# Performance work log

Hardware: AMD Instinct MI355X
Metric: run time of the kernel (lower is better)

Reference implementation:

```python
import jax, jax.numpy as jnp
import numpy as np

K = 16  # num_neighbors
L = 3   # stacked PointTransformer layers


def _mlp2(x, w1, b1, w2, b2):
    return jax.nn.relu(x @ w1 + b1) @ w2 + b2


def setup_inputs() -> dict:
    key = jax.random.key(0)
    ks = jax.random.split(key, 10)
    B, N, D = 2, 8192, 3
    HP, HA = 32, 12  # pos_mlp hidden, attn_mlp hidden (3*4)
    f = lambda k, shp, s: jax.random.normal(k, shp, dtype=jnp.float32) * s
    return {
        "feats": f(ks[0], (B, N, D), 1.0),
        "pos": f(ks[1], (B, N, 3), 1.0),
        "mask": jnp.ones((B, N), dtype=bool),  # unused by PT.forward
        "w_qkv": f(ks[2], (L, D, 3 * D), 1.0 / np.sqrt(D)),
        "pos_w1": f(ks[3], (L, 3, HP), 1.0 / np.sqrt(3.0)),
        "pos_b1": jnp.zeros((L, HP), jnp.float32),
        "pos_w2": f(ks[4], (L, HP, D), 1.0 / np.sqrt(HP)),
        "pos_b2": jnp.zeros((L, D), jnp.float32),
        "attn_w1": f(ks[5], (L, D, HA), 1.0 / np.sqrt(D)),
        "attn_b1": jnp.zeros((L, HA), jnp.float32),
        "attn_w2": f(ks[6], (L, HA, D), 1.0 / np.sqrt(HA)),
        "attn_b2": jnp.zeros((L, D), jnp.float32),
        "lin_w": f(ks[7], (D, 2), 1.0 / np.sqrt(D)),
        "lin_b": jnp.zeros((2,), jnp.float32),
    }


def reference(feats, pos, mask, w_qkv, pos_w1, pos_b1, pos_w2, pos_b2,
              attn_w1, attn_b1, attn_w2, attn_b2, lin_w, lin_b):
    # kNN indices from pairwise squared distances (monotonic in the norm the
    # original uses, so topk-smallest gives identical neighbor sets).
    sq = jnp.sum(pos * pos, axis=-1)                               # [B,N]
    d2 = sq[:, :, None] + sq[:, None, :] - 2.0 * jnp.einsum('bic,bjc->bij', pos, pos)
    _, idx = jax.lax.top_k(-d2, K)                                 # [B,N,K]

    gather = jax.vmap(lambda t, i: t[i])                           # [B,N,d],[B,N,K]->[B,N,K,d]
    pos_j = gather(pos, idx)                                       # [B,N,K,3]
    rel_pos = pos[:, :, None, :] - pos_j                           # [B,N,K,3]

    h = feats
    for l in range(L):
        qkv = h @ w_qkv[l]                                         # [B,N,9]
        q, k, v = jnp.split(qkv, 3, axis=-1)
        k_j = gather(k, idx)                                       # [B,N,K,3]
        v_j = gather(v, idx)
        rel_emb = _mlp2(rel_pos, pos_w1[l], pos_b1[l], pos_w2[l], pos_b2[l])
        qk_rel = q[:, :, None, :] - k_j
        sim = _mlp2(qk_rel + rel_emb, attn_w1[l], attn_b1[l], attn_w2[l], attn_b2[l])
        attn = jax.nn.softmax(sim, axis=-2)                        # softmax over neighbors
        agg = jnp.einsum('bijd,bijd->bid', attn, v_j + rel_emb)    # [B,N,3]
        h = jax.nn.sigmoid(agg)
    out = h @ lin_w + lin_b                                        # [B,N,2]
    return jax.nn.softmax(out, axis=2)
```

## Files before the change

kernel.cpp:

```cpp
#include <hip/hip_runtime.h>
#include <math.h>

#define N_PTS 8192
#define BATCH 2
#define KNB 16
#define NQ (BATCH * N_PTS)

#define H    0.35f
#define INVH (1.0f / 0.35f)
#define NC   30
#define LBOX (0.5f * H * NC)
#define NCELL (NC * NC * NC)
#define MCELL (2 * NCELL)
#define RMAXF 2
#define NCHK 8
#define CHKP (N_PTS / NCHK)
#define SCANG 8192
#define MERGG 1024
#define WCAP 8192

typedef unsigned long long u64;

__device__ __forceinline__ float med3f(float a, float b, float c) {
#if __has_builtin(__builtin_amdgcn_fmed3f)
    return __builtin_amdgcn_fmed3f(a, b, c);
#else
    return fmaxf(fminf(a, b), fminf(fmaxf(a, b), c));
#endif
}

__device__ __forceinline__ unsigned sortable(float x) {
    unsigned u = __float_as_uint(x);
    return u ^ ((unsigned)((int)u >> 31) | 0x80000000u);
}

__device__ __forceinline__ void ins_u64(u64 (&pk)[KNB], u64 key) {
    if (key < pk[0]) {
#pragma unroll
        for (int s = 0; s < KNB; ++s) {
            const u64 ds1 = (s < KNB - 1) ? pk[s + 1] : 0ull;
            const bool c0 = key < pk[s];
            const bool c1 = key < ds1;
            pk[s] = c1 ? ds1 : (c0 ? key : pk[s]);
        }
    }
}

__device__ __forceinline__ void sort16_desc_u64(u64 (&a)[KNB]) {
#pragma unroll
    for (int k = 2; k <= 16; k <<= 1) {
#pragma unroll
        for (int j = k >> 1; j > 0; j >>= 1) {
#pragma unroll
            for (int i = 0; i < 16; ++i) {
                const int l = i ^ j;
                if (l > i) {
                    const bool dirDesc = ((i & k) == 0);
                    const u64 mx = a[i] > a[l] ? a[i] : a[l];
                    const u64 mn = a[i] > a[l] ? a[l] : a[i];
                    a[i] = dirDesc ? mx : mn;
                    a[l] = dirDesc ? mn : mx;
                }
            }
        }
    }
}

__device__ __forceinline__ void merge64_u64(u64 (&pk)[KNB]) {
#pragma unroll
    for (int mm = 1; mm <= 32; mm <<= 1) {
        u64 L[KNB];
#pragma unroll
        for (int i = 0; i < KNB; ++i) {
            const u64 a = pk[i];
            const u64 c = __shfl_xor(pk[KNB - 1 - i], mm);
            L[i] = a < c ? a : c;
        }
#pragma unroll
        for (int dd = 8; dd >= 1; dd >>= 1) {
#pragma unroll
            for (int i = 0; i < KNB; ++i) {
                if ((i & dd) == 0) {
                    const u64 hi = L[i] > L[i | dd] ? L[i] : L[i | dd];
                    const u64 lo = L[i] > L[i | dd] ? L[i | dd] : L[i];
                    L[i] = hi; L[i | dd] = lo;
                }
            }
        }
#pragma unroll
        for (int i = 0; i < KNB; ++i) pk[i] = L[i];
    }
}

__global__ __launch_bounds__(256) void kzero(int* __restrict__ p, int n) {
    const int i = blockIdx.x * 256 + threadIdx.x;
    if (i < n) p[i] = 0;
}

__global__ __launch_bounds__(256) void kcount(const float* __restrict__ pos,
                                              int* __restrict__ cnt,
                                              int* __restrict__ cellid) {
    const int g = blockIdx.x * 256 + threadIdx.x;
    const int b = g >> 13;
    const float x = pos[g * 3 + 0], y = pos[g * 3 + 1], z = pos[g * 3 + 2];
    int cx = (int)floorf((x + LBOX) * INVH); cx = min(max(cx, 0), NC - 1);
    int cy = (int)floorf((y + LBOX) * INVH); cy = min(max(cy, 0), NC - 1);
    int cz = (int)floorf((z + LBOX) * INVH); cz = min(max(cz, 0), NC - 1);
    const int c = (((b * NC) + cz) * NC + cy) * NC + cx;
    cellid[g] = c;
    atomicAdd(&cnt[c], 1);
}

__global__ __launch_bounds__(1024) void kscan1(const int* __restrict__ cnt,
                                               int* __restrict__ scanned,
                                               int* __restrict__ bsum) {
    __shared__ int sh[1024];
    const int t = threadIdx.x;
    const int idx = blockIdx.x * 1024 + t;
    int v = (idx < MCELL) ? cnt[idx] : 0;
    sh[t] = v;
    __syncthreads();
    for (int off = 1; off < 1024; off <<= 1) {
        const int add = (t >= off) ? sh[t - off] : 0;
        __syncthreads();
        sh[t] += add;
        __syncthreads();
    }
    if (idx < MCELL) scanned[idx] = sh[t];
    if (t == 1023) bsum[blockIdx.x] = sh[1023];
}

__global__ __launch_bounds__(1024) void kscan2(const int* __restrict__ scanned,
                                               const int* __restrict__ bsum,
                                               int* __restrict__ cell_start) {
    __shared__ int soff;
    const int t = threadIdx.x;
    const int blk = blockIdx.x;
    const int idx = blk * 1024 + t;
    if (t == 0) {
        int s = 0;
        for (int k = 0; k < blk; ++k) s += bsum[k];
        soff = s;
    }
    __syncthreads();
    if (idx < MCELL) cell_start[idx + 1] = scanned[idx] + soff;
    if (idx == 0) cell_start[0] = 0;
}

__global__ __launch_bounds__(256) void kscatter(const float* __restrict__ pos,
                                                const int* __restrict__ cellid,
                                                const int* __restrict__ cell_start,
                                                int* __restrict__ cnt2,
                                                float4* __restrict__ spp,
                                                int* __restrict__ sidx) {
    const int g = blockIdx.x * 256 + threadIdx.x;
    const int c = cellid[g];
    const int off = atomicAdd(&cnt2[c], 1);
    const int p = cell_start[c] + off;
    const float x = pos[g * 3 + 0], y = pos[g * 3 + 1], z = pos[g * 3 + 2];
    spp[p] = make_float4(-2.f * x, -2.f * y, -2.f * z, fmaf(x, x, fmaf(y, y, z * z)));
    sidx[p] = g & (N_PTS - 1);
}

__global__ __launch_bounds__(64) void ksearch_fast(const float4* __restrict__ spp,
                                                   const int* __restrict__ sidx,
                                                   const int* __restrict__ cs,
                                                   int* __restrict__ knn,
                                                   int* __restrict__ ovf_list,
                                                   int* __restrict__ ovf_cnt) {
    const int tid = threadIdx.x;
    const int li  = tid & 15;
    const int sq  = blockIdx.x * 4 + (tid >> 4);
    const int b   = sq >> 13;

    const float4 me = spp[sq];
    const float qx = -0.5f * me.x, qy = -0.5f * me.y, qz = -0.5f * me.z;
    const float qsq = me.w;
    int cx = (int)floorf((qx + LBOX) * INVH); cx = min(max(cx, 0), NC - 1);
    int cy = (int)floorf((qy + LBOX) * INVH); cy = min(max(cy, 0), NC - 1);
    int cz = (int)floorf((qz + LBOX) * INVH); cz = min(max(cz, 0), NC - 1);

    auto do_ring = [&](int R, auto&& body) {
        const int zlo = max(cz - R, 0), zhi = min(cz + R, NC - 1);
        const int ylo = max(cy - R, 0), yhi = min(cy + R, NC - 1);
        const int xlo = max(cx - R, 0), xhi = min(cx + R, NC - 1);
        for (int z = zlo; z <= zhi; ++z) {
            const bool zf = (z == cz - R) || (z == cz + R);
            for (int y = ylo; y <= yhi; ++y) {
                const bool face = zf || (y == cy - R) || (y == cy + R);
                const int rowb = (((b * NC) + z) * NC + y) * NC;
                if (face) {
                    const int st = cs[rowb + xlo], en = cs[rowb + xhi + 1];
                    for (int p = st + li; p < en; p += 16) body(p);
                } else {
                    const int xm = cx - R, xp = cx + R;
                    if (xm >= 0) {
                        const int st = cs[rowb + xm], en = cs[rowb + xm + 1];
                        for (int p = st + li; p < en; p += 16) body(p);
                    }
                    if (xp < NC) {
                        const int st = cs[rowb + xp], en = cs[rowb + xp + 1];
                        for (int p = st + li; p < en; p += 16) body(p);
                    }
                }
            }
        }
    };

    float d[KNB];
#pragma unroll
    for (int k = 0; k < KNB; ++k) d[k] = 3.4e38f;

    auto scan1 = [&](int p) {
        const float4 v = spp[p];
        const float x = fmaf(qx, v.x, fmaf(qy, v.y, fmaf(qz, v.z, v.w)));
        if (x < d[0]) {
#pragma unroll
            for (int s = 0; s < KNB - 1; ++s) d[s] = med3f(d[s], d[s + 1], x);
            d[KNB - 1] = fminf(d[KNB - 1], x);
        }
    };

    int Rfin = -1;
    for (int R = 0; R <= RMAXF; ++R) {
        do_ring(R, scan1);
        const float bxl = fmaf((float)(cx - R), H, -LBOX);
        const float bxh = fmaf((float)(cx + R + 1), H, -LBOX);
        const float byl = fmaf((float)(cy - R), H, -LBOX);
        const float byh = fmaf((float)(cy + R + 1), H, -LBOX);
        const float bzl = fmaf((float)(cz - R), H, -LBOX);
        const float bzh = fmaf((float)(cz + R + 1), H, -LBOX);
        const float m = fminf(fminf(fminf(qx - bxl, bxh - qx),
                                    fminf(qy - byl, byh - qy)),
                              fminf(qz - bzl, bzh - qz));
        if (m > 0.f) {
            const float Bf = fmaf(m, m, -1e-4f) - qsq;
            int c = 0;
#pragma unroll
            for (int k = 0; k < KNB; ++k) c += (d[k] <= Bf) ? 1 : 0;
#pragma unroll
            for (int off = 1; off < 16; off <<= 1) c += __shfl_xor(c, off);
            if (c >= KNB) { Rfin = R; break; }
        }
    }

    if (Rfin < 0) {
        if (li == 0) { const int s2 = atomicAdd(ovf_cnt, 1); ovf_list[s2] = sq; }
        return;
    }

#pragma unroll
    for (int mm = 1; mm <= 8; mm <<= 1) {
        float L[KNB];
#pragma unroll
        for (int i = 0; i < KNB; ++i)
            L[i] = fminf(d[i], __shfl_xor(d[KNB - 1 - i], mm));
#pragma unroll
        for (int dd = 8; dd >= 1; dd >>= 1) {
#pragma unroll
            for (int i = 0; i < KNB; ++i) {
                if ((i & dd) == 0) {
                    const float hi = fmaxf(L[i], L[i | dd]);
                    const float lo = fminf(L[i], L[i | dd]);
                    L[i] = hi; L[i | dd] = lo;
                }
            }
        }
#pragma unroll
        for (int i = 0; i < KNB; ++i) d[i] = L[i];
    }
    const float thr = d[0];

    u64 pk[KNB];
#pragma unroll
    for (int k = 0; k < KNB; ++k) pk[k] = 0xFFFFFFFFFFFFFFFFull;

    auto scan2 = [&](int p) {
        const float4 v = spp[p];
        const float x = fmaf(qx, v.x, fmaf(qy, v.y, fmaf(qz, v.z, v.w)));
        if (x <= thr) {
            ins_u64(pk, ((u64)sortable(x) << 32) | (unsigned)sidx[p]);
        }
    };
    for (int R = 0; R <= Rfin; ++R) do_ring(R, scan2);

#pragma unroll
    for (int mm = 1; mm <= 8; mm <<= 1) {
        u64 L[KNB];
#pragma unroll
        for (int i = 0; i < KNB; ++i) {
            const u64 a = pk[i];
            const u64 c = __shfl_xor(pk[KNB - 1 - i], mm);
            L[i] = a < c ? a : c;
        }
#pragma unroll
        for (int dd = 8; dd >= 1; dd >>= 1) {
#pragma unroll
            for (int i = 0; i < KNB; ++i) {
                if ((i & dd) == 0) {
                    const u64 hi = L[i] > L[i | dd] ? L[i] : L[i | dd];
                    const u64 lo = L[i] > L[i | dd] ? L[i | dd] : L[i];
                    L[i] = hi; L[i | dd] = lo;
                }
            }
        }
#pragma unroll
        for (int i = 0; i < KNB; ++i) pk[i] = L[i];
    }

    const int qorig = sidx[sq];
    const int obase = ((b << 13) + qorig) * KNB;
    u64 sel = pk[0];
#pragma unroll
    for (int s = 1; s < KNB; ++s) sel = (li == s) ? pk[s] : sel;
    knn[obase + li] = (int)(unsigned)(sel & 0xFFFFFFFFull);
}

__global__ __launch_bounds__(64, 4) void kslow_scan(const float4* __restrict__ spp,
                                                    const int* __restrict__ sidx,
                                                    const int* __restrict__ ovf_list,
                                                    const int* __restrict__ ovf_cnt,
                                                    u64* __restrict__ pbuf) {
    const int lane = threadIdx.x;
    const int ntask = min(*ovf_cnt, WCAP) * NCHK;

    for (int task = blockIdx.x; task < ntask; task += SCANG) {
        const int w = task >> 3;
        const int c = task & (NCHK - 1);
        const int sq = ovf_list[w];
        const int b  = sq >> 13;
        const float4 me = spp[sq];
        const float qx = -0.5f * me.x, qy = -0.5f * me.y, qz = -0.5f * me.z;
        const int cbase = (b << 13) + c * CHKP;

        u64 pk[KNB];
#pragma unroll
        for (int t0 = 0; t0 < 2; ++t0) {
            const int tb = cbase + lane + t0 * 512;
            float4 v[8];
            int id[8];
#pragma unroll
            for (int u = 0; u < 8; ++u) v[u] = spp[tb + u * 64];
#pragma unroll
            for (int u = 0; u < 8; ++u) id[u] = sidx[tb + u * 64];
#pragma unroll
            for (int u = 0; u < 8; ++u) {
                const float x = fmaf(qx, v[u].x, fmaf(qy, v[u].y, fmaf(qz, v[u].z, v[u].w)));
                pk[t0 * 8 + u] = ((u64)sortable(x) << 32) | (unsigned)id[u];
            }
        }

        sort16_desc_u64(pk);
        merge64_u64(pk);

        u64 sel = pk[0];
#pragma unroll
        for (int s = 1; s < KNB; ++s) sel = (lane == s) ? pk[s] : sel;
        if (lane < KNB) pbuf[(size_t)task * KNB + lane] = sel;
    }
}

__global__ __launch_bounds__(64) void kslow_merge(const float4* __restrict__ spp,
                                                  const int* __restrict__ sidx,
                                                  int* __restrict__ knn,
                                                  const int* __restrict__ ovf_list,
                                                  const int* __restrict__ ovf_cnt,
                                                  const u64* __restrict__ pbuf) {
    const int lane = threadIdx.x;
    const int nov = *ovf_cnt;

    for (int w = blockIdx.x; w < nov; w += MERGG) {
        const int sq = ovf_list[w];
        const int b  = sq >> 13;

        u64 pk[KNB];
#pragma unroll
        for (int k = 0; k < KNB; ++k) pk[k] = 0xFFFFFFFFFFFFFFFFull;

        if (w < WCAP) {
            const u64 a0 = pbuf[(size_t)w * (NCHK * KNB) + lane];
            const u64 a1 = pbuf[(size_t)w * (NCHK * KNB) + 64 + lane];
            ins_u64(pk, a0);
            ins_u64(pk, a1);
        } else {
            const float4 me = spp[sq];
            const float qx = -0.5f * me.x, qy = -0.5f * me.y, qz = -0.5f * me.z;
            const int base = b << 13;
            unsigned smax = 0xFFFFFFFFu;
            for (int t = lane; t < N_PTS; t += 64) {
                const float4 v = spp[base + t];
                const float x = fmaf(qx, v.x, fmaf(qy, v.y, fmaf(qz, v.z, v.w)));
                const unsigned sx = sortable(x);
                if (sx <= smax) {
                    ins_u64(pk, ((u64)sx << 32) | (unsigned)sidx[base + t]);
                    smax = (unsigned)(pk[0] >> 32);
                }
            }
        }

        merge64_u64(pk);

        const int qorig = sidx[sq];
        const int obase = ((b << 13) + qorig) * KNB;
        u64 sel = pk[0];
#pragma unroll
        for (int s = 1; s < KNB; ++s) sel = (lane == s) ? pk[s] : sel;
        if (lane < KNB) knn[obase + lane] = (int)(unsigned)(sel & 0xFFFFFFFFull);
    }
}

__global__ __launch_bounds__(256) void pt_layer_f(const float* __restrict__ hin,
                                                  const float* __restrict__ pos,
                                                  const int* __restrict__ knn,
                                                  const float* __restrict__ wqkv,
                                                  const float* __restrict__ pw1,
                                                  const float* __restrict__ pb1,
                                                  const float* __restrict__ pw2,
                                                  const float* __restrict__ pb2,
                                                  const float* __restrict__ aw1,
                                                  const float* __restrict__ ab1,
                                                  const float* __restrict__ aw2,
                                                  const float* __restrict__ ab2,
                                                  float* __restrict__ hout,
                                                  const float* __restrict__ lw,
                                                  const float* __restrict__ lb,
                                                  float* __restrict__ out,
                                                  int last) {
    const int gt = blockIdx.x * 256 + threadIdx.x;
    const int qg = gt >> 4;
    const int j  = gt & 15;
    const int b  = qg >> 13;
    const int jj = knn[qg * KNB + j] & (N_PTS - 1);
    const int g  = (b << 13) + jj;

    const float hi0 = hin[qg * 3 + 0], hi1 = hin[qg * 3 + 1], hi2 = hin[qg * 3 + 2];
    const float hj0 = hin[g * 3 + 0],  hj1 = hin[g * 3 + 1],  hj2 = hin[g * 3 + 2];
    const float rx = pos[qg * 3 + 0] - pos[g * 3 + 0];
    const float ry = pos[qg * 3 + 1] - pos[g * 3 + 1];
    const float rz = pos[qg * 3 + 2] - pos[g * 3 + 2];

    const float q0 = fmaf(hi0, wqkv[0], fmaf(hi1, wqkv[9],  hi2 * wqkv[18]));
    const float q1 = fmaf(hi0, wqkv[1], fmaf(hi1, wqkv[10], hi2 * wqkv[19]));
    const float q2 = fmaf(hi0, wqkv[2], fmaf(hi1, wqkv[11], hi2 * wqkv[20]));
    const float k0 = fmaf(hj0, wqkv[3], fmaf(hj1, wqkv[12], hj2 * wqkv[21]));
    const float k1 = fmaf(hj0, wqkv[4], fmaf(hj1, wqkv[13], hj2 * wqkv[22]));
    const float k2 = fmaf(hj0, wqkv[5], fmaf(hj1, wqkv[14], hj2 * wqkv[23]));
    const float v0 = fmaf(hj0, wqkv[6], fmaf(hj1, wqkv[15], hj2 * wqkv[24]));
    const float v1 = fmaf(hj0, wqkv[7], fmaf(hj1, wqkv[16], hj2 * wqkv[25]));
    const float v2 = fmaf(hj0, wqkv[8], fmaf(hj1, wqkv[17], hj2 * wqkv[26]));

    float e0 = pb2[0], e1 = pb2[1], e2 = pb2[2];
#pragma unroll
    for (int hh = 0; hh < 32; ++hh) {
        float t = fmaf(rx, pw1[hh], fmaf(ry, pw1[32 + hh], fmaf(rz, pw1[64 + hh], pb1[hh])));
        t = fmaxf(t, 0.0f);
        e0 = fmaf(t, pw2[hh * 3 + 0], e0);
        e1 = fmaf(t, pw2[hh * 3 + 1], e1);
        e2 = fmaf(t, pw2[hh * 3 + 2], e2);
    }

    const float x0 = q0 - k0 + e0;
    const float x1 = q1 - k1 + e1;
    const float x2 = q2 - k2 + e2;

    float s0 = ab2[0], s1 = ab2[1], s2 = ab2[2];
#pragma unroll
    for (int hh = 0; hh < 12; ++hh) {
        float t = fmaf(x0, aw1[hh], fmaf(x1, aw1[12 + hh], fmaf(x2, aw1[24 + hh], ab1[hh])));
        t = fmaxf(t, 0.0f);
        s0 = fmaf(t, aw2[hh * 3 + 0], s0);
        s1 = fmaf(t, aw2[hh * 3 + 1], s1);
        s2 = fmaf(t, aw2[hh * 3 + 2], s2);
    }

    const float w0 = v0 + e0, w1 = v1 + e1, w2 = v2 + e2;

    float m0 = s0, m1 = s1, m2 = s2;
#pragma unroll
    for (int off = 1; off < 16; off <<= 1) {
        m0 = fmaxf(m0, __shfl_xor(m0, off));
        m1 = fmaxf(m1, __shfl_xor(m1, off));
        m2 = fmaxf(m2, __shfl_xor(m2, off));
    }
    const float ex0 = __expf(s0 - m0), ex1 = __expf(s1 - m1), ex2 = __expf(s2 - m2);
    float n0 = ex0 * w0, n1 = ex1 * w1, n2 = ex2 * w2;
    float den0 = ex0, den1 = ex1, den2 = ex2;
#pragma unroll
    for (int off = 1; off < 16; off <<= 1) {
        den0 += __shfl_xor(den0, off); n0 += __shfl_xor(n0, off);
        den1 += __shfl_xor(den1, off); n1 += __shfl_xor(n1, off);
        den2 += __shfl_xor(den2, off); n2 += __shfl_xor(n2, off);
    }

    if (j == 0) {
        const float h0 = 1.f / (1.f + __expf(-(n0 / den0)));
        const float h1 = 1.f / (1.f + __expf(-(n1 / den1)));
        const float h2 = 1.f / (1.f + __expf(-(n2 / den2)));
        if (!last) {
            hout[qg * 3 + 0] = h0;
            hout[qg * 3 + 1] = h1;
            hout[qg * 3 + 2] = h2;
        } else {
            const float o0 = fmaf(h0, lw[0], fmaf(h1, lw[2], fmaf(h2, lw[4], lb[0])));
            const float o1 = fmaf(h0, lw[1], fmaf(h1, lw[3], fmaf(h2, lw[5], lb[1])));
            const float mm = fmaxf(o0, o1);
            const float ea = __expf(o0 - mm), eb = __expf(o1 - mm);
            const float inv = 1.f / (ea + eb);
            out[qg * 2 + 0] = ea * inv;
            out[qg * 2 + 1] = eb * inv;
        }
    }
}

extern "C" void kernel_launch(void* const* d_in, const int* in_sizes, int n_in,
                              void* d_out, int out_size, void* d_ws, size_t ws_size,
                              hipStream_t stream) {
    const float* feats = (const float*)d_in[0];
    const float* pos   = (const float*)d_in[1];
    const float* wqkv = (const float*)d_in[3];
    const float* pw1  = (const float*)d_in[4];
    const float* pb1  = (const float*)d_in[5];
    const float* pw2  = (const float*)d_in[6];
    const float* pb2  = (const float*)d_in[7];
    const float* aw1  = (const float*)d_in[8];
    const float* ab1  = (const float*)d_in[9];
    const float* aw2  = (const float*)d_in[10];
    const float* ab2  = (const float*)d_in[11];
    const float* lw   = (const float*)d_in[12];
    const float* lb   = (const float*)d_in[13];
    float* out = (float*)d_out;

    size_t o = 0;
    auto take = [&](size_t bytes) { size_t r = o; o += (bytes + 15) & ~(size_t)15; return r; };
    const size_t o_cnt   = take((size_t)(2 * MCELL + 4) * 4);
    const size_t o_scan  = take((size_t)MCELL * 4);
    const size_t o_cs    = take((size_t)(MCELL + 1) * 4);
    const size_t o_bsum  = take((size_t)256 * 4);
    const size_t o_cid   = take((size_t)NQ * 4);
    const size_t o_spp   = take((size_t)NQ * 16);
    const size_t o_sidx  = take((size_t)NQ * 4);
    const size_t o_knn   = take((size_t)NQ * KNB * 4);
    const size_t o_ovfl  = take((size_t)NQ * 4);
    const size_t o_hA    = take((size_t)NQ * 3 * 4);
    const size_t o_hB    = take((size_t)NQ * 3 * 4);
    const size_t o_pbuf  = take((size_t)WCAP * NCHK * KNB * 8);
    if (ws_size < o) return;

    char* ws = (char*)d_ws;
    int*    cnt     = (int*)(ws + o_cnt);
    int*    cnt2    = cnt + MCELL;
    int*    ovf_cnt = cnt + 2 * MCELL;
    int*    scan  = (int*)(ws + o_scan);
    int*    cs    = (int*)(ws + o_cs);
    int*    bsum  = (int*)(ws + o_bsum);
    int*    cid   = (int*)(ws + o_cid);
    float4* spp   = (float4*)(ws + o_spp);
    int*    sidx  = (int*)(ws + o_sidx);
    int*    knn   = (int*)(ws + o_knn);
    int*    ovfl  = (int*)(ws + o_ovfl);
    float*  hA    = (float*)(ws + o_hA);
    float*  hB    = (float*)(ws + o_hB);
    u64*    pbuf  = (u64*)(ws + o_pbuf);

    const int nscan = (MCELL + 1023) / 1024;

    kzero<<<(2 * MCELL + 1 + 255) / 256, 256, 0, stream>>>(cnt, 2 * MCELL + 1);
    kcount<<<NQ / 256, 256, 0, stream>>>(pos, cnt, cid);
    kscan1<<<nscan, 1024, 0, stream>>>(cnt, scan, bsum);
    kscan2<<<nscan, 1024, 0, stream>>>(scan, bsum, cs);
    kscatter<<<NQ / 256, 256, 0, stream>>>(pos, cid, cs, cnt2, spp, sidx);
    ksearch_fast<<<NQ / 4, 64, 0, stream>>>(spp, sidx, cs, knn, ovfl, ovf_cnt);
    kslow_scan<<<SCANG, 64, 0, stream>>>(spp, sidx, ovfl, ovf_cnt, pbuf);
    kslow_merge<<<MERGG, 64, 0, stream>>>(spp, sidx, knn, ovfl, ovf_cnt, pbuf);

    pt_layer_f<<<NQ * 16 / 256, 256, 0, stream>>>(feats, pos, knn,
        wqkv + 0, pw1 + 0, pb1 + 0, pw2 + 0, pb2 + 0,
        aw1 + 0, ab1 + 0, aw2 + 0, ab2 + 0,
        hA, lw, lb, out, 0);
    pt_layer_f<<<NQ * 16 / 256, 256, 0, stream>>>(hA, pos, knn,
        wqkv + 27, pw1 + 96, pb1 + 32, pw2 + 96, pb2 + 3,
        aw1 + 36, ab1 + 12, aw2 + 36, ab2 + 3,
        hB, lw, lb, out, 0);
    pt_layer_f<<<NQ * 16 / 256, 256, 0, stream>>>(hB, pos, knn,
        wqkv + 54, pw1 + 192, pb1 + 64, pw2 + 192, pb2 + 6,
        aw1 + 72, ab1 + 24, aw2 + 72, ab2 + 6,
        hB, lw, lb, out, 1);
}
```

Before: 137.6 us.

## Precompute neighbor cell row ranges in shared memory for kNN search

The kNN search kernel now computes the start and end of each cell-row range for the 3x3x3 and 5x5x5 shells cooperatively, once per block, and stores them in shared memory. The scans then walk a flat list of rows instead of nested ring loops with face tests. Radius 0 is dropped and the search starts at radius 1, so the separate R=0 bound test is gone. The first-pass insert also loses its `x < d[0]` branch, so every candidate now runs the full med3 network. This trades divergent control flow and repeated cs loads for extra ALU work and a block-wide sync.

```diff
diff --git a/kernel.cpp b/kernel.cpp
--- a/kernel.cpp
+++ b/kernel.cpp
@@ -12,7 +12,8 @@
 #define LBOX (0.5f * H * NC)
 #define NCELL (NC * NC * NC)
 #define MCELL (2 * NCELL)
-#define RMAXF 2
+#define NROW1 9
+#define NROWT 43
 #define NCHK 8
 #define CHKP (N_PTS / NCHK)
 #define SCANG 8192
@@ -168,10 +169,59 @@
                                                    int* __restrict__ knn,
                                                    int* __restrict__ ovf_list,
                                                    int* __restrict__ ovf_cnt) {
+    __shared__ int rst[4][NROWT], ren[4][NROWT];
     const int tid = threadIdx.x;
     const int li  = tid & 15;
-    const int sq  = blockIdx.x * 4 + (tid >> 4);
+    const int gq  = tid >> 4;
+    const int sq  = blockIdx.x * 4 + gq;
     const int b   = sq >> 13;
+
+    for (int t = tid; t < 4 * NROWT; t += 64) {
+        const int q = t / NROWT, r = t % NROWT;
+        const int sq2 = blockIdx.x * 4 + q;
+        const int b2  = sq2 >> 13;
+        const float4 m2 = spp[sq2];
+        const float px = -0.5f * m2.x, py = -0.5f * m2.y, pz = -0.5f * m2.z;
+        int c2x = (int)floorf((px + LBOX) * INVH); c2x = min(max(c2x, 0), NC - 1);
+        int c2y = (int)floorf((py + LBOX) * INVH); c2y = min(max(c2y, 0), NC - 1);
+        int c2z = (int)floorf((pz + LBOX) * INVH); c2z = min(max(c2z, 0), NC - 1);
+
+        int st = 0, en = 0;
+        int z, y, xlo, xhi;
+        bool ok = true;
+        if (r < NROW1) {
+            z = c2z + r / 3 - 1;
+            y = c2y + (r % 3) - 1;
+            xlo = max(c2x - 1, 0); xhi = min(c2x + 1, NC - 1);
+        } else {
+            const int rr = r - NROW1;
+            if (rr < 10) {
+                z = c2z + (rr < 5 ? -2 : 2);
+                y = c2y + (rr % 5) - 2;
+                xlo = max(c2x - 2, 0); xhi = min(c2x + 2, NC - 1);
+            } else if (rr < 16) {
+                const int k = rr - 10;
+                z = c2z + (k % 3) - 1;
+                y = c2y + (k < 3 ? -2 : 2);
+                xlo = max(c2x - 2, 0); xhi = min(c2x + 2, NC - 1);
+            } else {
+                const int k = rr - 16;
+                const int m = k % 9;
+                z = c2z + m / 3 - 1;
+                y = c2y + (m % 3) - 1;
+                const int xx = c2x + (k < 9 ? -2 : 2);
+                xlo = xhi = xx;
+                ok = (xx >= 0) && (xx < NC);
+            }
+        }
+        if (ok && z >= 0 && z < NC && y >= 0 && y < NC) {
+            const int rowb = (((b2 * NC) + z) * NC + y) * NC;
+            st = cs[rowb + xlo];
+            en = cs[rowb + xhi + 1];
+        }
+        rst[q][r] = st; ren[q][r] = en;
+    }
+    __syncthreads();
 
     const float4 me = spp[sq];
     const float qx = -0.5f * me.x, qy = -0.5f * me.y, qz = -0.5f * me.z;
@@ -180,50 +230,24 @@
     int cy = (int)floorf((qy + LBOX) * INVH); cy = min(max(cy, 0), NC - 1);
     int cz = (int)floorf((qz + LBOX) * INVH); cz = min(max(cz, 0), NC - 1);
 
-    auto do_ring = [&](int R, auto&& body) {
-        const int zlo = max(cz - R, 0), zhi = min(cz + R, NC - 1);
-        const int ylo = max(cy - R, 0), yhi = min(cy + R, NC - 1);
-        const int xlo = max(cx - R, 0), xhi = min(cx + R, NC - 1);
-        for (int z = zlo; z <= zhi; ++z) {
-            const bool zf = (z == cz - R) || (z == cz + R);
-            for (int y = ylo; y <= yhi; ++y) {
-                const bool face = zf || (y == cy - R) || (y == cy + R);
-                const int rowb = (((b * NC) + z) * NC + y) * NC;
-                if (face) {
-                    const int st = cs[rowb + xlo], en = cs[rowb + xhi + 1];
-                    for (int p = st + li; p < en; p += 16) body(p);
-                } else {
-                    const int xm = cx - R, xp = cx + R;
-                    if (xm >= 0) {
-                        const int st = cs[rowb + xm], en = cs[rowb + xm + 1];
-                        for (int p = st + li; p < en; p += 16) body(p);
-                    }
-                    if (xp < NC) {
-                        const int st = cs[rowb + xp], en = cs[rowb + xp + 1];
-                        for (int p = st + li; p < en; p += 16) body(p);
-                    }
-                }
+    float d[KNB];
+#pragma unroll
+    for (int k = 0; k < KNB; ++k) d[k] = 3.4e38f;
+
+    auto scan1_rows = [&](int r0, int r1) {
+        for (int r = r0; r < r1; ++r) {
+            const int st = rst[gq][r], en = ren[gq][r];
+            for (int p = st + li; p < en; p += 16) {
+                const float4 v = spp[p];
+                const float x = fmaf(qx, v.x, fmaf(qy, v.y, fmaf(qz, v.z, v.w)));
+#pragma unroll
+                for (int s = 0; s < KNB - 1; ++s) d[s] = med3f(d[s], d[s + 1], x);
+                d[KNB - 1] = fminf(d[KNB - 1], x);
             }
         }
     };
 
-    float d[KNB];
-#pragma unroll
-    for (int k = 0; k < KNB; ++k) d[k] = 3.4e38f;
-
-    auto scan1 = [&](int p) {
-        const float4 v = spp[p];
-        const float x = fmaf(qx, v.x, fmaf(qy, v.y, fmaf(qz, v.z, v.w)));
-        if (x < d[0]) {
-#pragma unroll
-            for (int s = 0; s < KNB - 1; ++s) d[s] = med3f(d[s], d[s + 1], x);
-            d[KNB - 1] = fminf(d[KNB - 1], x);
-        }
-    };
-
-    int Rfin = -1;
-    for (int R = 0; R <= RMAXF; ++R) {
-        do_ring(R, scan1);
+    auto boundtest = [&](int R) -> bool {
         const float bxl = fmaf((float)(cx - R), H, -LBOX);
         const float bxh = fmaf((float)(cx + R + 1), H, -LBOX);
         const float byl = fmaf((float)(cy - R), H, -LBOX);
@@ -233,21 +257,28 @@
         const float m = fminf(fminf(fminf(qx - bxl, bxh - qx),
                                     fminf(qy - byl, byh - qy)),
                               fminf(qz - bzl, bzh - qz));
-        if (m > 0.f) {
-            const float Bf = fmaf(m, m, -1e-4f) - qsq;
-            int c = 0;
-#pragma unroll
-            for (int k = 0; k < KNB; ++k) c += (d[k] <= Bf) ? 1 : 0;
-#pragma unroll
-            for (int off = 1; off < 16; off <<= 1) c += __shfl_xor(c, off);
-            if (c >= KNB) { Rfin = R; break; }
-        }
-    }
-
-    if (Rfin < 0) {
+        if (!(m > 0.f)) return false;
+        const float Bf = fmaf(m, m, -1e-4f) - qsq;
+        int c = 0;
+#pragma unroll
+        for (int k = 0; k < KNB; ++k) c += (d[k] <= Bf) ? 1 : 0;
+#pragma unroll
+        for (int off = 1; off < 16; off <<= 1) c += __shfl_xor(c, off);
+        return c >= KNB;
+    };
+
+    scan1_rows(0, NROW1);
+    const bool done1 = boundtest(1);
+    bool ovf = false;
+    if (!done1) {
+        scan1_rows(NROW1, NROWT);
+        if (!boundtest(2)) ovf = true;
+    }
+    if (ovf) {
         if (li == 0) { const int s2 = atomicAdd(ovf_cnt, 1); ovf_list[s2] = sq; }
         return;
     }
+    const int nrows = done1 ? NROW1 : NROWT;
 
 #pragma unroll
     for (int mm = 1; mm <= 8; mm <<= 1) {
@@ -275,14 +306,16 @@
 #pragma unroll
     for (int k = 0; k < KNB; ++k) pk[k] = 0xFFFFFFFFFFFFFFFFull;
 
-    auto scan2 = [&](int p) {
-        const float4 v = spp[p];
-        const float x = fmaf(qx, v.x, fmaf(qy, v.y, fmaf(qz, v.z, v.w)));
-        if (x <= thr) {
-            ins_u64(pk, ((u64)sortable(x) << 32) | (unsigned)sidx[p]);
-        }
-    };
-    for (int R = 0; R <= Rfin; ++R) do_ring(R, scan2);
+    for (int r = 0; r < nrows; ++r) {
+        const int st = rst[gq][r], en = ren[gq][r];
+        for (int p = st + li; p < en; p += 16) {
+            const float4 v = spp[p];
+            const float x = fmaf(qx, v.x, fmaf(qy, v.y, fmaf(qz, v.z, v.w)));
+            if (x <= thr) {
+                ins_u64(pk, ((u64)sortable(x) << 32) | (unsigned)sidx[p]);
+            }
+        }
+    }
 
 #pragma unroll
     for (int mm = 1; mm <= 8; mm <<= 1) {
```

New measurement: 125.6 us. -8.8%, faster.
